# Kernel optimization log

Hardware: AMD Instinct MI355X
Metric: run time of the kernel (lower is better)

Reference implementation:

```python
import jax, jax.numpy as jnp
import numpy as np

B, N, C, H, W = 16, 64, 128, 64, 64
IMG = 512.0
SCALE = 0.125          # spatial_scale
MAX_GRID = 16          # >= ceil(max_roi_side * SCALE); boxes built so sides <= 128px -> 16
OUT_CH = 256


def setup_inputs() -> dict:
    key = jax.random.key(0)
    k1, k2, k3, k4, k5 = jax.random.split(key, 5)
    z = jax.random.normal(k1, (B, C, H, W), jnp.float32)
    xy = jax.random.uniform(k2, (B, N, 2), jnp.float32, 0.0, IMG - 128.0)
    wh = jax.random.uniform(k3, (B, N, 2), jnp.float32, 8.0, 128.0)
    bboxes = jnp.concatenate([xy, xy + wh], axis=-1)  # [B,N,4] xyxy, image coords
    W_out = jax.random.normal(k4, (OUT_CH, C), jnp.float32) / np.sqrt(C).astype(np.float32)
    b_out = jax.random.normal(k5, (OUT_CH,), jnp.float32) * 0.01
    return {"z": z, "bboxes": bboxes, "W_out": W_out, "b_out": b_out}


def _prep_coord(c, L):
    # torchvision bilinear edge handling; c: sample coord, L: spatial extent
    inr = (c > -1.0) & (c < float(L))          # out of range -> value 0 (still counted)
    cc = jnp.clip(c, 0.0, None)
    lo = jnp.minimum(jnp.floor(cc).astype(jnp.int32), L - 1)
    hi = jnp.minimum(lo + 1, L - 1)
    cc = jnp.where(lo >= L - 1, lo.astype(c.dtype), cc)
    frac = cc - lo.astype(c.dtype)
    return lo, hi, frac, inr


def roi_align_1x1(z, boxes, scale=SCALE, max_grid=MAX_GRID):
    # z: [B,C,H,W], boxes: [B,N,4] xyxy. torchvision roi_align, output_size=1,
    # aligned=True, sampling_ratio=-1 (adaptive grid = ceil(roi_side), masked to max_grid).
    Bz, Cz, Hh, Ww = z.shape
    b = boxes * scale - 0.5                       # aligned=True offset
    x1, y1, x2, y2 = b[..., 0], b[..., 1], b[..., 2], b[..., 3]
    roi_w, roi_h = x2 - x1, y2 - y1               # [B,N]
    gw = jnp.clip(jnp.ceil(roi_w), 1.0, float(max_grid))
    gh = jnp.clip(jnp.ceil(roi_h), 1.0, float(max_grid))
    g = jnp.arange(max_grid, dtype=z.dtype)
    sy = y1[..., None] + (g + 0.5) * (roi_h / gh)[..., None]   # [B,N,G]
    sx = x1[..., None] + (g + 0.5) * (roi_w / gw)[..., None]
    vy = g < gh[..., None]                        # grid-validity (adaptive count)
    vx = g < gw[..., None]

    yl, yh, fy, iry = _prep_coord(sy, Hh)
    xl, xh, fx, irx = _prep_coord(sx, Ww)
    hy, hx = 1.0 - fy, 1.0 - fx

    zf = z.transpose(0, 2, 3, 1)                  # [B,H,W,C]
    shp = (Bz, boxes.shape[1], max_grid, max_grid)
    Yl = jnp.broadcast_to(yl[..., :, None], shp)
    Yh = jnp.broadcast_to(yh[..., :, None], shp)
    Xl = jnp.broadcast_to(xl[..., None, :], shp)
    Xh = jnp.broadcast_to(xh[..., None, :], shp)

    gather = jax.vmap(lambda zb, yi, xi: zb[yi, xi])   # -> [B,N,G,G,C]
    v11 = gather(zf, Yl, Xl)
    v12 = gather(zf, Yl, Xh)
    v21 = gather(zf, Yh, Xl)
    v22 = gather(zf, Yh, Xh)

    w11 = hy[..., :, None] * hx[..., None, :]
    w12 = hy[..., :, None] * fx[..., None, :]
    w21 = fy[..., :, None] * hx[..., None, :]
    w22 = fy[..., :, None] * fx[..., None, :]
    val = (w11[..., None] * v11 + w12[..., None] * v12
           + w21[..., None] * v21 + w22[..., None] * v22)   # [B,N,G,G,C]

    mask = ((vy[..., :, None] & vx[..., None, :])
            & (iry[..., :, None] & irx[..., None, :])).astype(z.dtype)
    val = val * mask[..., None]
    count = (gh * gw)[..., None]                   # adaptive sample count
    return val.sum(axis=(2, 3)) / count            # [B,N,C]


def reference(z, bboxes, W_out, b_out):
    # roi_align (output 1x1) -> avgpool(1) is identity -> reshape [B,N,C] -> Linear
    feats = roi_align_1x1(z, bboxes)               # [B,N,C]
    return feats @ W_out.T + b_out                 # [B,N,OUT_CH]
```

## Files before the change

### kernel.cpp

```cpp
#include <hip/hip_runtime.h>
#include <hip/hip_bf16.h>

#define B_ 16
#define N_ 64
#define C_ 128
#define H_ 64
#define W_ 64
#define HW_ (H_ * W_)
#define OUT_CH_ 256
#define MAX_GRID_ 16
#define SCALE_ 0.125f

__device__ __forceinline__ unsigned int packbf2(float lo, float hi) {
  __hip_bfloat162 h = __float22bfloat162_rn(float2{lo, hi});
  return *(unsigned int*)&h;
}

__global__ __launch_bounds__(256) void transpose_kernel(
    const float* __restrict__ z, const float* __restrict__ Wm,
    unsigned int* __restrict__ zf, float* __restrict__ Wt) {
  __shared__ unsigned int tile32[128 * 65];
  const int t = threadIdx.x;

  if (blockIdx.y == 16) {
    float* ft = (float*)tile32;
    int x  = blockIdx.x;
    int ot = x & 7, ct = x >> 3;
    int j = t & 31, i0 = t >> 5;
#pragma unroll
    for (int k = 0; k < 4; ++k) {
      int i = i0 + k * 8;
      ft[i * 33 + j] = Wm[(size_t)(ot * 32 + i) * C_ + ct * 32 + j];
    }
    __syncthreads();
#pragma unroll
    for (int k = 0; k < 4; ++k) {
      int i = i0 + k * 8;
      Wt[(size_t)(ct * 32 + i) * OUT_CH_ + ot * 32 + j] = ft[j * 33 + i];
    }
    return;
  }

  const int b  = blockIdx.y;
  const int pt = blockIdx.x;
  const float* zb = z + (size_t)b * C_ * HW_ + pt * 128;
#pragma unroll
  for (int iter = 0; iter < 8; ++iter) {
    int idx = iter * 256 + t;
    int c2  = idx >> 5;
    int p4  = (idx & 31) << 2;
    const float* r0 = zb + (size_t)(c2 * 2) * HW_ + p4;
    float4 a = *(const float4*)r0;
    float4 c = *(const float4*)(r0 + HW_);
    tile32[(p4 + 0) * 65 + c2] = packbf2(a.x, c.x);
    tile32[(p4 + 1) * 65 + c2] = packbf2(a.y, c.y);
    tile32[(p4 + 2) * 65 + c2] = packbf2(a.z, c.z);
    tile32[(p4 + 3) * 65 + c2] = packbf2(a.w, c.w);
  }
  __syncthreads();

  unsigned int* zfb = zf + (size_t)b * HW_ * 64 + (size_t)pt * 128 * 64;
#pragma unroll
  for (int iter = 0; iter < 8; ++iter) {
    int idx = iter * 256 + t;
    int p   = idx >> 4;
    int q   = (idx & 15) << 2;
    uint4 u = *(const uint4*)&tile32[p * 65 + q];
    *(uint4*)(zfb + (size_t)p * 64 + q) = u;
  }
}

__global__ __launch_bounds__(512) void roi_fused_kernel(
    const unsigned int* __restrict__ zf,
    const float* __restrict__ boxes,
    const float* __restrict__ Wt,
    const float* __restrict__ bias,
    float* __restrict__ out)
{
  int bid = blockIdx.x;
  int img = (bid & 7) | ((bid >> 9) << 3);
  int roi = img * N_ + ((bid >> 3) & 63);
  int t   = threadIdx.x;
  int wv  = t >> 6;
  int c2  = t & 63;

  float4 bx = ((const float4*)boxes)[roi];
  float x1 = bx.x * SCALE_ - 0.5f;
  float y1 = bx.y * SCALE_ - 0.5f;
  float roi_w = bx.z * SCALE_ - 0.5f - x1;
  float roi_h = bx.w * SCALE_ - 0.5f - y1;
  float gwf = fminf(fmaxf(ceilf(roi_w), 1.0f), (float)MAX_GRID_);
  float ghf = fminf(fmaxf(ceilf(roi_h), 1.0f), (float)MAX_GRID_);
  int gw = (int)gwf;
  int gh = (int)ghf;
  float stepx = roi_w / gwf;
  float stepy = roi_h / ghf;

  const unsigned int* zb = zf + (size_t)img * (HW_ * 64) + c2;

  float acc0 = 0.0f, acc1 = 0.0f;
  for (int gy = wv; gy < gh; gy += 8) {
    float sy = y1 + ((float)gy + 0.5f) * stepy;
    float wy = (sy > -1.0f && sy < (float)H_) ? 1.0f : 0.0f;
    float cy = fmaxf(sy, 0.0f);
    int yl = (int)cy;
    yl = yl < (H_ - 1) ? yl : (H_ - 1);
    int yh = (yl + 1) < (H_ - 1) ? (yl + 1) : (H_ - 1);
    if (yl >= H_ - 1) cy = (float)yl;
    float fy = cy - (float)yl;
    float hy = 1.0f - fy;
    const unsigned int* rowl = zb + (size_t)yl * (W_ * 64);
    const unsigned int* rowh = zb + (size_t)yh * (W_ * 64);

    float nfx, nhx, nm;
    int nxl, nxh;
    {
      float sx = x1 + 0.5f * stepx;
      float wx = (sx > -1.0f && sx < (float)W_) ? 1.0f : 0.0f;
      float cx = fmaxf(sx, 0.0f);
      int xl = (int)cx;
      xl = xl < (W_ - 1) ? xl : (W_ - 1);
      int xh = (xl + 1) < (W_ - 1) ? (xl + 1) : (W_ - 1);
      if (xl >= W_ - 1) cx = (float)xl;
      nfx = cx - (float)xl; nhx = 1.0f - nfx; nm = wy * wx;
      nxl = xl; nxh = xh;
    }
    unsigned int n11 = rowl[nxl << 6], n12 = rowl[nxh << 6];
    unsigned int n21 = rowh[nxl << 6], n22 = rowh[nxh << 6];

    for (int gx = 0; gx < gw; ++gx) {
      unsigned int v11 = n11, v12 = n12, v21 = n21, v22 = n22;
      float fx = nfx, hx = nhx, m = nm;

      int ngx = (gx + 1 < gw) ? gx + 1 : gx;
      {
        float sx = x1 + ((float)ngx + 0.5f) * stepx;
        float wx = (sx > -1.0f && sx < (float)W_) ? 1.0f : 0.0f;
        float cx = fmaxf(sx, 0.0f);
        int xl = (int)cx;
        xl = xl < (W_ - 1) ? xl : (W_ - 1);
        int xh = (xl + 1) < (W_ - 1) ? (xl + 1) : (W_ - 1);
        if (xl >= W_ - 1) cx = (float)xl;
        nfx = cx - (float)xl; nhx = 1.0f - nfx; nm = wy * wx;
        nxl = xl; nxh = xh;
      }
      n11 = rowl[nxl << 6]; n12 = rowl[nxh << 6];
      n21 = rowh[nxl << 6]; n22 = rowh[nxh << 6];

      float w11 = hy * hx * m, w12 = hy * fx * m;
      float w21 = fy * hx * m, w22 = fy * fx * m;
      acc0 += w11 * __uint_as_float(v11 << 16)
            + w12 * __uint_as_float(v12 << 16)
            + w21 * __uint_as_float(v21 << 16)
            + w22 * __uint_as_float(v22 << 16);
      acc1 += w11 * __uint_as_float(v11 & 0xffff0000u)
            + w12 * __uint_as_float(v12 & 0xffff0000u)
            + w21 * __uint_as_float(v21 & 0xffff0000u)
            + w22 * __uint_as_float(v22 & 0xffff0000u);
    }
  }

  __shared__ float red[8][128];
  __shared__ float feat[128];
  __shared__ float lin[2][256];
  int co = c2 << 1;
  red[wv][co]     = acc0;
  red[wv][co + 1] = acc1;
  __syncthreads();
  if (t < 128) {
    float s = (red[0][t] + red[1][t]) + (red[2][t] + red[3][t])
            + (red[4][t] + red[5][t]) + (red[6][t] + red[7][t]);
    feat[t] = s * (1.0f / (ghf * gwf));
  }
  __syncthreads();

  int oc   = t & 255;
  int half = t >> 8;
  const float* wp = Wt + (size_t)(half * 64) * OUT_CH_ + oc;
  const float* fp = feat + half * 64;
  float a = 0.0f;
#pragma unroll 8
  for (int k = 0; k < 64; ++k)
    a += fp[k] * wp[(size_t)k * OUT_CH_];
  lin[half][oc] = a;
  __syncthreads();
  if (t < 256)
    out[(size_t)roi * OUT_CH_ + t] = lin[0][t] + lin[1][t] + bias[t];
}

extern "C" void kernel_launch(void* const* d_in, const int* in_sizes, int n_in,
                              void* d_out, int out_size, void* d_ws, size_t ws_size,
                              hipStream_t stream) {
  const float* z     = (const float*)d_in[0];
  const float* boxes = (const float*)d_in[1];
  const float* Wm    = (const float*)d_in[2];
  const float* bias  = (const float*)d_in[3];
  float* out = (float*)d_out;

  char* ws = (char*)d_ws;
  unsigned int* zf = (unsigned int*)ws;
  float* Wt = (float*)(ws + (size_t)B_ * HW_ * C_ * 2);

  transpose_kernel<<<dim3(HW_ / 128, B_ + 1), 256, 0, stream>>>(z, Wm, zf, Wt);
  roi_fused_kernel<<<B_ * N_, 512, 0, stream>>>(zf, boxes, Wt, bias, out);
}
```

Before: 100.6 us.

## Precompute bilinear sample metadata in LDS and split wavefronts across x-samples

Per-sample x/y indices and edge-masked weights are now computed once per ROI into shared-memory tables instead of being recomputed in every thread's inner loop. Each wavefront is split into two half-waves that handle alternating x samples, and each lane loads 4 bf16 channels (uint2) per corner instead of 2. This is meant to cut redundant address and weight arithmetic and to halve the number of load instructions per sample. The cost is an extra barrier, a 16-way LDS reduction, and idle half-waves when the grid width is odd.

```diff
diff --git a/kernel.cpp b/kernel.cpp
--- a/kernel.cpp
+++ b/kernel.cpp
@@ -82,7 +82,9 @@
   int roi = img * N_ + ((bid >> 3) & 63);
   int t   = threadIdx.x;
   int wv  = t >> 6;
-  int c2  = t & 63;
+  int lane = t & 63;
+  int half = lane >> 5;
+  int cq   = lane & 31;
 
   float4 bx = ((const float4*)boxes)[roi];
   float x1 = bx.x * SCALE_ - 0.5f;
@@ -96,93 +98,106 @@
   float stepx = roi_w / gwf;
   float stepy = roi_h / ghf;
 
-  const unsigned int* zb = zf + (size_t)img * (HW_ * 64) + c2;
-
-  float acc0 = 0.0f, acc1 = 0.0f;
-  for (int gy = wv; gy < gh; gy += 8) {
-    float sy = y1 + ((float)gy + 0.5f) * stepy;
-    float wy = (sy > -1.0f && sy < (float)H_) ? 1.0f : 0.0f;
+  __shared__ float4 xmeta[16];
+  __shared__ float4 ymeta[16];
+  if (t < 16) {
+    int g = t;
+    float sx = x1 + ((float)g + 0.5f) * stepx;
+    float v  = (g < gw && sx > -1.0f && sx < (float)W_) ? 1.0f : 0.0f;
+    float cx = fmaxf(sx, 0.0f);
+    int xl = (int)cx;
+    xl = xl < (W_ - 1) ? xl : (W_ - 1);
+    int xh = (xl + 1) < (W_ - 1) ? (xl + 1) : (W_ - 1);
+    if (xl >= W_ - 1) cx = (float)xl;
+    float fx = cx - (float)xl;
+    float4 m;
+    m.x = __int_as_float(xl << 6);
+    m.y = __int_as_float(xh << 6);
+    m.z = (1.0f - fx) * v;
+    m.w = fx * v;
+    xmeta[g] = m;
+  } else if (t >= 64 && t < 80) {
+    int g = t - 64;
+    float sy = y1 + ((float)g + 0.5f) * stepy;
+    float v  = (g < gh && sy > -1.0f && sy < (float)H_) ? 1.0f : 0.0f;
     float cy = fmaxf(sy, 0.0f);
     int yl = (int)cy;
     yl = yl < (H_ - 1) ? yl : (H_ - 1);
     int yh = (yl + 1) < (H_ - 1) ? (yl + 1) : (H_ - 1);
     if (yl >= H_ - 1) cy = (float)yl;
     float fy = cy - (float)yl;
-    float hy = 1.0f - fy;
-    const unsigned int* rowl = zb + (size_t)yl * (W_ * 64);
-    const unsigned int* rowh = zb + (size_t)yh * (W_ * 64);
-
-    float nfx, nhx, nm;
-    int nxl, nxh;
-    {
-      float sx = x1 + 0.5f * stepx;
-      float wx = (sx > -1.0f && sx < (float)W_) ? 1.0f : 0.0f;
-      float cx = fmaxf(sx, 0.0f);
-      int xl = (int)cx;
-      xl = xl < (W_ - 1) ? xl : (W_ - 1);
-      int xh = (xl + 1) < (W_ - 1) ? (xl + 1) : (W_ - 1);
-      if (xl >= W_ - 1) cx = (float)xl;
-      nfx = cx - (float)xl; nhx = 1.0f - nfx; nm = wy * wx;
-      nxl = xl; nxh = xh;
+    float4 m;
+    m.x = __int_as_float(yl * (W_ * 64));
+    m.y = __int_as_float(yh * (W_ * 64));
+    m.z = (1.0f - fy) * v;
+    m.w = fy * v;
+    ymeta[g] = m;
+  }
+  __syncthreads();
+
+  const unsigned int* zb = zf + (size_t)img * (HW_ * 64) + (cq << 1);
+
+  float a0 = 0.0f, a1 = 0.0f, a2 = 0.0f, a3 = 0.0f;
+  for (int gy = wv; gy < gh; gy += 8) {
+    float4 ym = ymeta[gy];
+    int yloff = __float_as_int(ym.x);
+    int yhoff = __float_as_int(ym.y);
+    float ah = ym.z, af = ym.w;
+
+    for (int gxp = 0; gxp < gw; gxp += 2) {
+      int gx = gxp + half;
+      float4 xm = xmeta[gx];
+      int xloff = __float_as_int(xm.x);
+      int xhoff = __float_as_int(xm.y);
+      float w11 = ah * xm.z, w12 = ah * xm.w;
+      float w21 = af * xm.z, w22 = af * xm.w;
+
+      uint2 v11 = *(const uint2*)(zb + yloff + xloff);
+      uint2 v12 = *(const uint2*)(zb + yloff + xhoff);
+      uint2 v21 = *(const uint2*)(zb + yhoff + xloff);
+      uint2 v22 = *(const uint2*)(zb + yhoff + xhoff);
+
+      a0 += w11 * __uint_as_float(v11.x << 16)
+          + w12 * __uint_as_float(v12.x << 16)
+          + w21 * __uint_as_float(v21.x << 16)
+          + w22 * __uint_as_float(v22.x << 16);
+      a1 += w11 * __uint_as_float(v11.x & 0xffff0000u)
+          + w12 * __uint_as_float(v12.x & 0xffff0000u)
+          + w21 * __uint_as_float(v21.x & 0xffff0000u)
+          + w22 * __uint_as_float(v22.x & 0xffff0000u);
+      a2 += w11 * __uint_as_float(v11.y << 16)
+          + w12 * __uint_as_float(v12.y << 16)
+          + w21 * __uint_as_float(v21.y << 16)
+          + w22 * __uint_as_float(v22.y << 16);
+      a3 += w11 * __uint_as_float(v11.y & 0xffff0000u)
+          + w12 * __uint_as_float(v12.y & 0xffff0000u)
+          + w21 * __uint_as_float(v21.y & 0xffff0000u)
+          + w22 * __uint_as_float(v22.y & 0xffff0000u);
     }
-    unsigned int n11 = rowl[nxl << 6], n12 = rowl[nxh << 6];
-    unsigned int n21 = rowh[nxl << 6], n22 = rowh[nxh << 6];
-
-    for (int gx = 0; gx < gw; ++gx) {
-      unsigned int v11 = n11, v12 = n12, v21 = n21, v22 = n22;
-      float fx = nfx, hx = nhx, m = nm;
-
-      int ngx = (gx + 1 < gw) ? gx + 1 : gx;
-      {
-        float sx = x1 + ((float)ngx + 0.5f) * stepx;
-        float wx = (sx > -1.0f && sx < (float)W_) ? 1.0f : 0.0f;
-        float cx = fmaxf(sx, 0.0f);
-        int xl = (int)cx;
-        xl = xl < (W_ - 1) ? xl : (W_ - 1);
-        int xh = (xl + 1) < (W_ - 1) ? (xl + 1) : (W_ - 1);
-        if (xl >= W_ - 1) cx = (float)xl;
-        nfx = cx - (float)xl; nhx = 1.0f - nfx; nm = wy * wx;
-        nxl = xl; nxh = xh;
-      }
-      n11 = rowl[nxl << 6]; n12 = rowl[nxh << 6];
-      n21 = rowh[nxl << 6]; n22 = rowh[nxh << 6];
-
-      float w11 = hy * hx * m, w12 = hy * fx * m;
-      float w21 = fy * hx * m, w22 = fy * fx * m;
-      acc0 += w11 * __uint_as_float(v11 << 16)
-            + w12 * __uint_as_float(v12 << 16)
-            + w21 * __uint_as_float(v21 << 16)
-            + w22 * __uint_as_float(v22 << 16);
-      acc1 += w11 * __uint_as_float(v11 & 0xffff0000u)
-            + w12 * __uint_as_float(v12 & 0xffff0000u)
-            + w21 * __uint_as_float(v21 & 0xffff0000u)
-            + w22 * __uint_as_float(v22 & 0xffff0000u);
-    }
-  }
-
-  __shared__ float red[8][128];
+  }
+
+  __shared__ float red[16][128];
   __shared__ float feat[128];
   __shared__ float lin[2][256];
-  int co = c2 << 1;
-  red[wv][co]     = acc0;
-  red[wv][co + 1] = acc1;
+  *(float4*)&red[wv * 2 + half][cq << 2] = float4{a0, a1, a2, a3};
   __syncthreads();
   if (t < 128) {
-    float s = (red[0][t] + red[1][t]) + (red[2][t] + red[3][t])
-            + (red[4][t] + red[5][t]) + (red[6][t] + red[7][t]);
+    float s = 0.0f;
+#pragma unroll
+    for (int r = 0; r < 16; ++r) s += red[r][t];
     feat[t] = s * (1.0f / (ghf * gwf));
   }
   __syncthreads();
 
-  int oc   = t & 255;
-  int half = t >> 8;
-  const float* wp = Wt + (size_t)(half * 64) * OUT_CH_ + oc;
-  const float* fp = feat + half * 64;
+  int oc = t & 255;
+  int hk = t >> 8;
+  const float* wp = Wt + (size_t)(hk * 64) * OUT_CH_ + oc;
+  const float* fp = feat + hk * 64;
   float a = 0.0f;
 #pragma unroll 8
   for (int k = 0; k < 64; ++k)
     a += fp[k] * wp[(size_t)k * OUT_CH_];
-  lin[half][oc] = a;
+  lin[hk][oc] = a;
   __syncthreads();
   if (t < 256)
     out[(size_t)roi * OUT_CH_ + t] = lin[0][t] + lin[1][t] + bias[t];
```

Result: faster. 97.01 us (median of 2 runs) (-3.5%).
